# Performance work log

Measured on AMD Instinct MI355X. Metric: run time of the kernel, lower is better.

The kernel has to match this reference:

```python
import jax, jax.numpy as jnp
import numpy as np

N = 100000
E = 2000000
F = 64          # in_features == out_features (required by attention * h_j)
BETA = 0.5
NEG_SLOPE = 0.01  # torch F.leaky_relu default


def setup_inputs() -> dict:
    key = jax.random.key(0)
    k1, k2, k3, k4, k5, k6 = jax.random.split(key, 6)
    h = jax.random.normal(k1, (N, F), dtype=jnp.float32)
    adj = jax.random.randint(k2, (2, E), 0, N, dtype=jnp.int64)
    amount = jax.random.uniform(k3, (E,), dtype=jnp.float32)
    count = jax.random.uniform(k4, (E,), dtype=jnp.float32)
    fc_w = jax.random.normal(k5, (F, 2 * F), dtype=jnp.float32) * (1.0 / np.sqrt(2 * F))
    fc_b = jax.random.normal(k6, (F,), dtype=jnp.float32) * 0.01
    return {"h": h, "adj": adj, "amount": amount, "count": count,
            "fc_w": fc_w, "fc_b": fc_b}


def _minmax_norm(x):
    lo, hi = x.min(), x.max()
    return (x - lo) / (hi - lo + 1e-8)


def reference(h, adj, amount, count, fc_w, fc_b):
    # per-edge weight from normalized amount/count
    edge_weight = BETA * _minmax_norm(amount) + (1.0 - BETA) * _minmax_norm(count)  # [E]

    src, dst = adj[0], adj[1]
    h_i = h[src]                     # [E, F]
    h_j = h[dst]                     # [E, F]
    h_cat = jnp.concatenate([h_i, h_j], axis=1)  # [E, 2F]

    score = jnp.einsum('ef,of->eo', h_cat, fc_w) + fc_b  # [E, F_out]
    score = jnp.where(score >= 0, score, NEG_SLOPE * score)  # leaky_relu
    score = score * edge_weight[:, None]

    # softmax over ALL edges (dim 0), per feature, as in the original
    attention = jax.nn.softmax(score, axis=0)  # [E, F]

    agg = jnp.zeros_like(h).at[src].add(attention * h_j)  # scatter-add -> [N, F]
    return agg
```

## Files before the change

kernel.cpp:

```cpp
#include <hip/hip_runtime.h>
#include <hip/hip_fp16.h>
#include <math.h>

#define FDIM   64
#define NB     128
#define BSHIFT 8
#define BMASK  255
#define EPTA   16
#define CHUNKA (EPTA * 256)
#define DMASK  0xFFFFF
#define MAXBKT 512

__global__ __launch_bounds__(256) void count_mm_k(const int* __restrict__ src,
                                                  const float* __restrict__ amount,
                                                  const float* __restrict__ count,
                                                  int* __restrict__ bktTotal,
                                                  float4* __restrict__ partial,
                                                  int E, int nbkt) {
  __shared__ int lhist[MAXBKT];
  __shared__ float4 lred[4];
  for (int k = threadIdx.x; k < nbkt; k += 256) lhist[k] = 0;
  __syncthreads();
  float amin = 3.4e38f, amax = -3.4e38f, cmin = 3.4e38f, cmax = -3.4e38f;
  int e0 = blockIdx.x * CHUNKA + threadIdx.x * EPTA;
  if (e0 + EPTA <= E) {
    #pragma unroll
    for (int q = 0; q < EPTA; q += 4) {
      int4   s4 = *(const int4*)(src + e0 + q);
      float4 a4 = *(const float4*)(amount + e0 + q);
      float4 c4 = *(const float4*)(count + e0 + q);
      atomicAdd(&lhist[s4.x >> BSHIFT], 1);
      atomicAdd(&lhist[s4.y >> BSHIFT], 1);
      atomicAdd(&lhist[s4.z >> BSHIFT], 1);
      atomicAdd(&lhist[s4.w >> BSHIFT], 1);
      amin = fminf(amin, fminf(fminf(a4.x, a4.y), fminf(a4.z, a4.w)));
      amax = fmaxf(amax, fmaxf(fmaxf(a4.x, a4.y), fmaxf(a4.z, a4.w)));
      cmin = fminf(cmin, fminf(fminf(c4.x, c4.y), fminf(c4.z, c4.w)));
      cmax = fmaxf(cmax, fmaxf(fmaxf(c4.x, c4.y), fmaxf(c4.z, c4.w)));
    }
  } else {
    for (int e = e0; e < E; e++) {
      atomicAdd(&lhist[src[e] >> BSHIFT], 1);
      float a = amount[e], c = count[e];
      amin = fminf(amin, a); amax = fmaxf(amax, a);
      cmin = fminf(cmin, c); cmax = fmaxf(cmax, c);
    }
  }
  #pragma unroll
  for (int off = 32; off; off >>= 1) {
    amin = fminf(amin, __shfl_down(amin, off));
    amax = fmaxf(amax, __shfl_down(amax, off));
    cmin = fminf(cmin, __shfl_down(cmin, off));
    cmax = fmaxf(cmax, __shfl_down(cmax, off));
  }
  if ((threadIdx.x & 63) == 0) lred[threadIdx.x >> 6] = make_float4(amin, amax, cmin, cmax);
  __syncthreads();
  for (int k = threadIdx.x; k < nbkt; k += 256)
    if (lhist[k]) atomicAdd(&bktTotal[k], lhist[k]);
  if (threadIdx.x == 0) {
    float4 r = lred[0];
    #pragma unroll
    for (int w = 1; w < 4; w++) {
      r.x = fminf(r.x, lred[w].x); r.y = fmaxf(r.y, lred[w].y);
      r.z = fminf(r.z, lred[w].z); r.w = fmaxf(r.w, lred[w].w);
    }
    partial[blockIdx.x] = r;
  }
}

__global__ __launch_bounds__(256) void scanB_k(const int* __restrict__ bktTotal,
                                               int* __restrict__ bbase,
                                               int* __restrict__ cursor,
                                               const float4* __restrict__ partial,
                                               float* __restrict__ mmf,
                                               int nbkt, int nb, int E) {
  __shared__ int lds[MAXBKT];
  const int t = threadIdx.x;
  for (int k = t; k < nbkt; k += 256) lds[k] = bktTotal[k];
  __syncthreads();
  __shared__ int tmp[256];
  int running = 0;
  for (int c0 = 0; c0 < nbkt; c0 += 256) {
    int x = (c0 + t < nbkt) ? lds[c0 + t] : 0;
    tmp[t] = x; __syncthreads();
    for (int off = 1; off < 256; off <<= 1) {
      int v = (t >= off) ? tmp[t - off] : 0;
      __syncthreads();
      tmp[t] += v; __syncthreads();
    }
    if (c0 + t < nbkt) {
      int b = running + tmp[t] - x;
      bbase[c0 + t] = b;
      cursor[c0 + t] = b;
    }
    running += tmp[255];
    __syncthreads();
  }
  if (t == 0) bbase[nbkt] = E;
  float amin = 3.4e38f, amax = -3.4e38f, cmin = 3.4e38f, cmax = -3.4e38f;
  for (int i = t; i < nb; i += 256) {
    float4 p = partial[i];
    amin = fminf(amin, p.x); amax = fmaxf(amax, p.y);
    cmin = fminf(cmin, p.z); cmax = fmaxf(cmax, p.w);
  }
  #pragma unroll
  for (int off = 32; off; off >>= 1) {
    amin = fminf(amin, __shfl_down(amin, off));
    amax = fmaxf(amax, __shfl_down(amax, off));
    cmin = fminf(cmin, __shfl_down(cmin, off));
    cmax = fmaxf(cmax, __shfl_down(cmax, off));
  }
  __shared__ float4 lred[4];
  if ((t & 63) == 0) lred[t >> 6] = make_float4(amin, amax, cmin, cmax);
  __syncthreads();
  if (t == 0) {
    float4 r = lred[0];
    #pragma unroll
    for (int w = 1; w < 4; w++) {
      r.x = fminf(r.x, lred[w].x); r.y = fmaxf(r.y, lred[w].y);
      r.z = fminf(r.z, lred[w].z); r.w = fmaxf(r.w, lred[w].w);
    }
    mmf[0] = r.x; mmf[1] = r.y; mmf[2] = r.z; mmf[3] = r.w;
  }
}

__global__ __launch_bounds__(256) void scatter_k(const int* __restrict__ src,
                                                 const int* __restrict__ dst,
                                                 const float* __restrict__ amount,
                                                 const float* __restrict__ count,
                                                 const float* __restrict__ mmf,
                                                 int* __restrict__ cursor,
                                                 int2* __restrict__ payload,
                                                 int E, int nbkt) {
  __shared__ int lhist[MAXBKT];
  __shared__ int lcur[MAXBKT];
  const int t = threadIdx.x;
  for (int k = t; k < nbkt; k += 256) lhist[k] = 0;
  __syncthreads();
  const float amin = mmf[0], amax = mmf[1], cmin = mmf[2], cmax = mmf[3];
  const float L2E = 1.4426950408889634f;
  const float ascale = 0.5f * L2E / (amax - amin + 1e-8f);
  const float cscale = 0.5f * L2E / (cmax - cmin + 1e-8f);
  int e0 = blockIdx.x * CHUNKA + t * EPTA;
  const bool full = (e0 + EPTA <= E);
  int4 S[4]; int4 D[4]; float4 A[4]; float4 C[4];
  if (full) {
    #pragma unroll
    for (int q = 0; q < 4; q++) {
      S[q] = *(const int4*)(src + e0 + 4 * q);
      D[q] = *(const int4*)(dst + e0 + 4 * q);
      A[q] = *(const float4*)(amount + e0 + 4 * q);
      C[q] = *(const float4*)(count + e0 + 4 * q);
      atomicAdd(&lhist[S[q].x >> BSHIFT], 1);
      atomicAdd(&lhist[S[q].y >> BSHIFT], 1);
      atomicAdd(&lhist[S[q].z >> BSHIFT], 1);
      atomicAdd(&lhist[S[q].w >> BSHIFT], 1);
    }
  } else {
    for (int e = e0; e < E; e++) atomicAdd(&lhist[src[e] >> BSHIFT], 1);
  }
  __syncthreads();
  for (int k = t; k < nbkt; k += 256)
    lcur[k] = lhist[k] ? atomicAdd(&cursor[k], lhist[k]) : 0;
  __syncthreads();
  auto ins = [&](int s, int d, float a, float c) {
    int b = s >> BSHIFT;
    float ew = (a - amin) * ascale + (c - cmin) * cscale;
    int pos = atomicAdd(&lcur[b], 1);
    payload[pos] = make_int2(d | ((s & BMASK) << 20), __float_as_int(ew));
  };
  if (full) {
    #pragma unroll
    for (int q = 0; q < 4; q++) {
      ins(S[q].x, D[q].x, A[q].x, C[q].x);
      ins(S[q].y, D[q].y, A[q].y, C[q].y);
      ins(S[q].z, D[q].z, A[q].z, C[q].z);
      ins(S[q].w, D[q].w, A[q].w, C[q].w);
    }
  } else {
    for (int e = e0; e < E; e++) ins(src[e], dst[e], amount[e], count[e]);
  }
}

__global__ __launch_bounds__(256) void binB_k(const int2* __restrict__ payload,
                                              const int* __restrict__ bbase,
                                              int2* __restrict__ edge_s,
                                              int E, int nbkt) {
  __shared__ int fcnt[256];
  __shared__ int tmp[256];
  __shared__ int fcur[256];
  const int b = blockIdx.x;
  const int t = threadIdx.x;
  const int base = bbase[b];
  const int end  = bbase[b + 1];
  fcnt[t] = 0;
  __syncthreads();
  for (int i = base + t; i < end; i += 256)
    atomicAdd(&fcnt[(payload[i].x >> 20) & BMASK], 1);
  __syncthreads();
  int x = fcnt[t];
  tmp[t] = x; __syncthreads();
  for (int off = 1; off < 256; off <<= 1) {
    int v = (t >= off) ? tmp[t - off] : 0;
    __syncthreads();
    tmp[t] += v; __syncthreads();
  }
  fcur[t] = base + tmp[t] - x;
  __syncthreads();
  for (int i = base + t; i < end; i += 256) {
    int2 v = payload[i];
    int pos = atomicAdd(&fcur[(v.x >> 20) & BMASK], 1);
    edge_s[pos] = v;
  }
}

__global__ __launch_bounds__(256) void pre_gemm(const float* __restrict__ h,
                                                const float* __restrict__ fc_w,
                                                const float* __restrict__ fc_b,
                                                float* __restrict__ G1,
                                                __half2* __restrict__ P, int N) {
  __shared__ float hs[NB * FDIM];
  const int t = threadIdx.x;
  const int o = t & 63, half = (t >> 6) & 1, rg = t >> 7;
  float w[FDIM];
  const float* wrow = fc_w + o * 128 + half * 64;
  #pragma unroll
  for (int f = 0; f < FDIM; f += 4) {
    float4 v = *(const float4*)(wrow + f);
    w[f] = v.x; w[f + 1] = v.y; w[f + 2] = v.z; w[f + 3] = v.w;
  }
  const float bias = (half == 0) ? fc_b[o] : 0.0f;
  const int n0 = blockIdx.x * NB;
  const int nrows = min(NB, N - n0);
  {
    const float4* hsrc = (const float4*)(h + (size_t)n0 * FDIM);
    float4* hd = (float4*)hs;
    for (int i = t; i < nrows * (FDIM / 4); i += 256) hd[i] = hsrc[i];
  }
  __syncthreads();
  const int r0 = rg * 64;
  const int r1 = min(r0 + 64, nrows);
  for (int n = r0; n < r1; n++) {
    float acc = bias;
    #pragma unroll
    for (int f = 0; f < FDIM; f += 4) {
      float4 hv = *(const float4*)(&hs[n * FDIM + f]);
      acc += hv.x * w[f] + hv.y * w[f + 1] + hv.z * w[f + 2] + hv.w * w[f + 3];
    }
    if (half == 0) {
      G1[(size_t)(n0 + n) * FDIM + o] = acc;
    } else {
      P[(size_t)(n0 + n) * FDIM + o] =
          __halves2half2(__float2half(acc), __float2half(hs[n * FDIM + o]));
    }
  }
}

__device__ __forceinline__ float2 unpack_h2(unsigned u) {
  __half2 v = *(__half2*)&u;
  return make_float2(__low2float(v), __high2float(v));
}

__global__ __launch_bounds__(256) void fused_k(const int2* __restrict__ edge_s,
                                               const int* __restrict__ bbase,
                                               const float* __restrict__ G1,
                                               const unsigned* __restrict__ P,
                                               double* __restrict__ colsum,
                                               float* __restrict__ out,
                                               int E, int nbkt) {
  const int lane = threadIdx.x & 63;
  const int wv = __builtin_amdgcn_readfirstlane(threadIdx.x >> 6);
  const int wid = blockIdx.x * 4 + wv;
  const int nw = gridDim.x * 4;
  float csum = 0.0f;
  const int per = (((E + nw - 1) / nw) + 63) & ~63;
  const int e0 = wid * per;
  const int e1 = min(e0 + per, E);
  if (e0 < E) {
    int lo = 0, hi = nbkt - 1;
    while (lo < hi) {
      int mid = (lo + hi + 1) >> 1;
      if (bbase[mid] <= e0) lo = mid; else hi = mid - 1;
    }
    int bkt = lo;
    int nextb = bbase[bkt + 1];
    int curnode = -1;
    bool firstf = true;
    float acc = 0.0f, g1 = 0.0f;
    auto flush_to = [&](int node) {
      if (curnode >= 0) {
        float* dp = out + (size_t)curnode * FDIM + lane;
        if (firstf) { atomicAdd(dp, acc); firstf = false; }
        else *dp = acc;
      }
      curnode = node; acc = 0.0f;
      g1 = G1[(size_t)node * FDIM + lane];
    };
    for (int c0 = e0; c0 < e1; c0 += 64) {
      const int m = min(64, e1 - c0);
      int2 p = make_int2(0, 0);
      if (lane < m) p = edge_s[c0 + lane];
      if (m == 64) {
        #pragma unroll 1
        for (int j = 0; j < 64; j += 16) {
          int dd[16], nd[16]; float ee[16]; unsigned uu[16];
          #pragma unroll
          for (int k = 0; k < 16; k++) {
            int x = __builtin_amdgcn_readlane(p.x, j + k);
            ee[k] = __int_as_float(__builtin_amdgcn_readlane(p.y, j + k));
            dd[k] = x & DMASK;
            nd[k] = (x >> 20) & BMASK;
          }
          #pragma unroll
          for (int k = 0; k < 16; k++) uu[k] = P[(size_t)dd[k] * FDIM + lane];
          #pragma unroll
          for (int k = 0; k < 16; k++) {
            int i = c0 + j + k;
            while (i >= nextb) { bkt++; nextb = bbase[bkt + 1]; }
            int node = (bkt << BSHIFT) + nd[k];
            if (node != curnode) flush_to(node);
            float2 v = unpack_h2(uu[k]);
            float sc = g1 + v.x;
            sc = fmaxf(sc, 0.01f * sc);
            float x = exp2f(sc * ee[k]);
            csum += x;
            acc += x * v.y;
          }
        }
      } else {
        for (int j = 0; j < m; j += 16) {
          const int rem = m - j;
          int dd[16], nd[16]; float ee[16]; unsigned uu[16];
          #pragma unroll
          for (int k = 0; k < 16; k++) {
            int x = __builtin_amdgcn_readlane(p.x, j + k);
            ee[k] = __int_as_float(__builtin_amdgcn_readlane(p.y, j + k));
            dd[k] = x & DMASK;
            nd[k] = (x >> 20) & BMASK;
          }
          #pragma unroll
          for (int k = 0; k < 16; k++) uu[k] = P[(size_t)dd[k] * FDIM + lane];
          #pragma unroll
          for (int k = 0; k < 16; k++) {
            if (k < rem) {
              int i = c0 + j + k;
              while (i >= nextb) { bkt++; nextb = bbase[bkt + 1]; }
              int node = (bkt << BSHIFT) + nd[k];
              if (node != curnode) flush_to(node);
              float2 v = unpack_h2(uu[k]);
              float sc = g1 + v.x;
              sc = fmaxf(sc, 0.01f * sc);
              float x = exp2f(sc * ee[k]);
              csum += x;
              acc += x * v.y;
            }
          }
        }
      }
    }
    if (curnode >= 0) atomicAdd(out + (size_t)curnode * FDIM + lane, acc);
  }
  __shared__ float part[256];
  part[threadIdx.x] = csum;
  __syncthreads();
  if (threadIdx.x < 64) {
    float tot = part[threadIdx.x] + part[threadIdx.x + 64] +
                part[threadIdx.x + 128] + part[threadIdx.x + 192];
    atomicAdd(&colsum[threadIdx.x * 16], (double)tot);
  }
}

__global__ __launch_bounds__(256) void scale_k(float4* __restrict__ out4,
                                               const double* __restrict__ colsum,
                                               int total4) {
  __shared__ float rinv_s[64];
  if (threadIdx.x < 64) rinv_s[threadIdx.x] = (float)(1.0 / colsum[threadIdx.x * 16]);
  __syncthreads();
  const float4* r4 = (const float4*)rinv_s;
  int idx = blockIdx.x * blockDim.x + threadIdx.x;
  int stride = gridDim.x * blockDim.x;
  for (int i = idx; i < total4; i += stride) {
    float4 v = out4[i];
    float4 r = r4[i & 15];
    v.x *= r.x; v.y *= r.y; v.z *= r.z; v.w *= r.w;
    out4[i] = v;
  }
}

extern "C" void kernel_launch(void* const* d_in, const int* in_sizes, int n_in,
                              void* d_out, int out_size, void* d_ws, size_t ws_size,
                              hipStream_t stream) {
  const float* h      = (const float*)d_in[0];
  const int*   adj    = (const int*)d_in[1];
  const float* amount = (const float*)d_in[2];
  const float* count  = (const float*)d_in[3];
  const float* fc_w   = (const float*)d_in[4];
  const float* fc_b   = (const float*)d_in[5];
  float* out = (float*)d_out;

  const int E = in_sizes[2];
  const int N = in_sizes[0] / FDIM;
  const int* src = adj;
  const int* dst = adj + E;
  const int nbkt  = (N + BMASK) >> BSHIFT;
  const int nblkA = (E + CHUNKA - 1) / CHUNKA;

  char* ws = (char*)d_ws;
  size_t off = 0;
  auto alloc = [&](size_t bytes) { void* p = ws + off; off += (bytes + 255) & ~(size_t)255; return p; };
  float*    G1       = (float*)alloc((size_t)N * FDIM * sizeof(float));
  __half2*  P        = (__half2*)alloc((size_t)N * FDIM * sizeof(__half2));
  int2*     edge_s   = (int2*)alloc((size_t)E * sizeof(int2));
  int2*     payload  = (int2*)alloc((size_t)E * sizeof(int2));
  char*     ctrl     = (char*)alloc(MAXBKT * sizeof(int) + 1024 * sizeof(double));
  int*      bktTotal = (int*)ctrl;
  double*   colsum   = (double*)(ctrl + MAXBKT * sizeof(int));
  int*      bbase    = (int*)alloc((MAXBKT + 1) * sizeof(int));
  int*      cursor   = (int*)alloc(MAXBKT * sizeof(int));
  float4*   mmpart   = (float4*)alloc((size_t)nblkA * sizeof(float4));
  float*    mmf      = (float*)alloc(4 * sizeof(float));

  hipMemsetAsync(d_out, 0, (size_t)out_size * sizeof(float), stream);
  hipMemsetAsync(ctrl, 0, MAXBKT * sizeof(int) + 1024 * sizeof(double), stream);
  count_mm_k<<<nblkA, 256, 0, stream>>>(src, amount, count, bktTotal, mmpart, E, nbkt);
  scanB_k<<<1, 256, 0, stream>>>(bktTotal, bbase, cursor, mmpart, mmf, nbkt, nblkA, E);
  scatter_k<<<nblkA, 256, 0, stream>>>(src, dst, amount, count, mmf, cursor, payload, E, nbkt);
  binB_k<<<nbkt, 256, 0, stream>>>(payload, bbase, edge_s, E, nbkt);
  pre_gemm<<<(N + NB - 1) / NB, 256, 0, stream>>>(h, fc_w, fc_b, G1, P, N);
  fused_k<<<4096, 256, 0, stream>>>(edge_s, bbase, G1, (const unsigned*)P, colsum, out, E, nbkt);
  scale_k<<<1024, 256, 0, stream>>>((float4*)out, colsum, N * FDIM / 4);
}
```

Measured before the change: 314.2 us.

## Fuse preprocessing into a cooperative kernel and merge binning with pre-GEMM

Replaces the two memsets and the count, scan and scatter kernels with one cooperative kernel that uses grid-wide syncs between phases. The edge data is loaded once and kept in registers across the histogram and scatter phases, so it is no longer re-read. The bucket binning and the pre-GEMM become one launch whose blocks take one role or the other by index. This cuts launch overhead and redundant reads, at the cost of grid.sync latency and a requirement that all nblkA (about 489) blocks be co-resident for the cooperative launch.

```diff
diff --git a/kernel.cpp b/kernel.cpp
--- a/kernel.cpp
+++ b/kernel.cpp
@@ -1,6 +1,9 @@
 #include <hip/hip_runtime.h>
+#include <hip/hip_cooperative_groups.h>
 #include <hip/hip_fp16.h>
 #include <math.h>
+
+namespace cg = cooperative_groups;
 
 #define FDIM   64
 #define NB     128
@@ -11,137 +14,43 @@
 #define DMASK  0xFFFFF
 #define MAXBKT 512
 
-__global__ __launch_bounds__(256) void count_mm_k(const int* __restrict__ src,
-                                                  const float* __restrict__ amount,
-                                                  const float* __restrict__ count,
-                                                  int* __restrict__ bktTotal,
-                                                  float4* __restrict__ partial,
-                                                  int E, int nbkt) {
-  __shared__ int lhist[MAXBKT];
-  __shared__ float4 lred[4];
-  for (int k = threadIdx.x; k < nbkt; k += 256) lhist[k] = 0;
-  __syncthreads();
-  float amin = 3.4e38f, amax = -3.4e38f, cmin = 3.4e38f, cmax = -3.4e38f;
-  int e0 = blockIdx.x * CHUNKA + threadIdx.x * EPTA;
-  if (e0 + EPTA <= E) {
-    #pragma unroll
-    for (int q = 0; q < EPTA; q += 4) {
-      int4   s4 = *(const int4*)(src + e0 + q);
-      float4 a4 = *(const float4*)(amount + e0 + q);
-      float4 c4 = *(const float4*)(count + e0 + q);
-      atomicAdd(&lhist[s4.x >> BSHIFT], 1);
-      atomicAdd(&lhist[s4.y >> BSHIFT], 1);
-      atomicAdd(&lhist[s4.z >> BSHIFT], 1);
-      atomicAdd(&lhist[s4.w >> BSHIFT], 1);
-      amin = fminf(amin, fminf(fminf(a4.x, a4.y), fminf(a4.z, a4.w)));
-      amax = fmaxf(amax, fmaxf(fmaxf(a4.x, a4.y), fmaxf(a4.z, a4.w)));
-      cmin = fminf(cmin, fminf(fminf(c4.x, c4.y), fminf(c4.z, c4.w)));
-      cmax = fmaxf(cmax, fmaxf(fmaxf(c4.x, c4.y), fmaxf(c4.z, c4.w)));
-    }
-  } else {
-    for (int e = e0; e < E; e++) {
-      atomicAdd(&lhist[src[e] >> BSHIFT], 1);
-      float a = amount[e], c = count[e];
-      amin = fminf(amin, a); amax = fmaxf(amax, a);
-      cmin = fminf(cmin, c); cmax = fmaxf(cmax, c);
-    }
-  }
-  #pragma unroll
-  for (int off = 32; off; off >>= 1) {
-    amin = fminf(amin, __shfl_down(amin, off));
-    amax = fmaxf(amax, __shfl_down(amax, off));
-    cmin = fminf(cmin, __shfl_down(cmin, off));
-    cmax = fmaxf(cmax, __shfl_down(cmax, off));
-  }
-  if ((threadIdx.x & 63) == 0) lred[threadIdx.x >> 6] = make_float4(amin, amax, cmin, cmax);
-  __syncthreads();
-  for (int k = threadIdx.x; k < nbkt; k += 256)
-    if (lhist[k]) atomicAdd(&bktTotal[k], lhist[k]);
-  if (threadIdx.x == 0) {
-    float4 r = lred[0];
-    #pragma unroll
-    for (int w = 1; w < 4; w++) {
-      r.x = fminf(r.x, lred[w].x); r.y = fmaxf(r.y, lred[w].y);
-      r.z = fminf(r.z, lred[w].z); r.w = fmaxf(r.w, lred[w].w);
-    }
-    partial[blockIdx.x] = r;
-  }
-}
-
-__global__ __launch_bounds__(256) void scanB_k(const int* __restrict__ bktTotal,
+__global__ __launch_bounds__(256) void build_k(const int* __restrict__ src,
+                                               const int* __restrict__ dst,
+                                               const float* __restrict__ amount,
+                                               const float* __restrict__ count,
+                                               float* __restrict__ out,
+                                               int* __restrict__ bktTotal,
+                                               double* __restrict__ colsum,
                                                int* __restrict__ bbase,
                                                int* __restrict__ cursor,
-                                               const float4* __restrict__ partial,
+                                               float4* __restrict__ partial,
                                                float* __restrict__ mmf,
-                                               int nbkt, int nb, int E) {
-  __shared__ int lds[MAXBKT];
-  const int t = threadIdx.x;
-  for (int k = t; k < nbkt; k += 256) lds[k] = bktTotal[k];
-  __syncthreads();
-  __shared__ int tmp[256];
-  int running = 0;
-  for (int c0 = 0; c0 < nbkt; c0 += 256) {
-    int x = (c0 + t < nbkt) ? lds[c0 + t] : 0;
-    tmp[t] = x; __syncthreads();
-    for (int off = 1; off < 256; off <<= 1) {
-      int v = (t >= off) ? tmp[t - off] : 0;
-      __syncthreads();
-      tmp[t] += v; __syncthreads();
-    }
-    if (c0 + t < nbkt) {
-      int b = running + tmp[t] - x;
-      bbase[c0 + t] = b;
-      cursor[c0 + t] = b;
-    }
-    running += tmp[255];
-    __syncthreads();
-  }
-  if (t == 0) bbase[nbkt] = E;
-  float amin = 3.4e38f, amax = -3.4e38f, cmin = 3.4e38f, cmax = -3.4e38f;
-  for (int i = t; i < nb; i += 256) {
-    float4 p = partial[i];
-    amin = fminf(amin, p.x); amax = fmaxf(amax, p.y);
-    cmin = fminf(cmin, p.z); cmax = fmaxf(cmax, p.w);
-  }
-  #pragma unroll
-  for (int off = 32; off; off >>= 1) {
-    amin = fminf(amin, __shfl_down(amin, off));
-    amax = fmaxf(amax, __shfl_down(amax, off));
-    cmin = fminf(cmin, __shfl_down(cmin, off));
-    cmax = fmaxf(cmax, __shfl_down(cmax, off));
-  }
-  __shared__ float4 lred[4];
-  if ((t & 63) == 0) lred[t >> 6] = make_float4(amin, amax, cmin, cmax);
-  __syncthreads();
-  if (t == 0) {
-    float4 r = lred[0];
-    #pragma unroll
-    for (int w = 1; w < 4; w++) {
-      r.x = fminf(r.x, lred[w].x); r.y = fmaxf(r.y, lred[w].y);
-      r.z = fminf(r.z, lred[w].z); r.w = fmaxf(r.w, lred[w].w);
-    }
-    mmf[0] = r.x; mmf[1] = r.y; mmf[2] = r.z; mmf[3] = r.w;
-  }
-}
-
-__global__ __launch_bounds__(256) void scatter_k(const int* __restrict__ src,
-                                                 const int* __restrict__ dst,
-                                                 const float* __restrict__ amount,
-                                                 const float* __restrict__ count,
-                                                 const float* __restrict__ mmf,
-                                                 int* __restrict__ cursor,
-                                                 int2* __restrict__ payload,
-                                                 int E, int nbkt) {
+                                               int2* __restrict__ payload,
+                                               int E, int N, int nbkt, int nblkA) {
+  cg::grid_group grid = cg::this_grid();
   __shared__ int lhist[MAXBKT];
   __shared__ int lcur[MAXBKT];
+  __shared__ int tmp[256];
+  __shared__ float4 lred[4];
   const int t = threadIdx.x;
+  const int gtid = blockIdx.x * 256 + t;
+  const int nthr = gridDim.x * 256;
+
+  {
+    float4* o4 = (float4*)out;
+    const int tot4 = N * FDIM / 4;
+    const float4 z = make_float4(0.f, 0.f, 0.f, 0.f);
+    for (int i = gtid; i < tot4; i += nthr) o4[i] = z;
+    if (blockIdx.x == 0) {
+      for (int k = t; k < nbkt; k += 256) bktTotal[k] = 0;
+      for (int k = t; k < 1024; k += 256) colsum[k] = 0.0;
+    }
+  }
   for (int k = t; k < nbkt; k += 256) lhist[k] = 0;
-  __syncthreads();
-  const float amin = mmf[0], amax = mmf[1], cmin = mmf[2], cmax = mmf[3];
-  const float L2E = 1.4426950408889634f;
-  const float ascale = 0.5f * L2E / (amax - amin + 1e-8f);
-  const float cscale = 0.5f * L2E / (cmax - cmin + 1e-8f);
-  int e0 = blockIdx.x * CHUNKA + t * EPTA;
+  grid.sync();
+
+  float amin = 3.4e38f, amax = -3.4e38f, cmin = 3.4e38f, cmax = -3.4e38f;
+  const int e0 = blockIdx.x * CHUNKA + t * EPTA;
   const bool full = (e0 + EPTA <= E);
   int4 S[4]; int4 D[4]; float4 A[4]; float4 C[4];
   if (full) {
@@ -155,17 +64,98 @@
       atomicAdd(&lhist[S[q].y >> BSHIFT], 1);
       atomicAdd(&lhist[S[q].z >> BSHIFT], 1);
       atomicAdd(&lhist[S[q].w >> BSHIFT], 1);
+      amin = fminf(amin, fminf(fminf(A[q].x, A[q].y), fminf(A[q].z, A[q].w)));
+      amax = fmaxf(amax, fmaxf(fmaxf(A[q].x, A[q].y), fmaxf(A[q].z, A[q].w)));
+      cmin = fminf(cmin, fminf(fminf(C[q].x, C[q].y), fminf(C[q].z, C[q].w)));
+      cmax = fmaxf(cmax, fmaxf(fmaxf(C[q].x, C[q].y), fmaxf(C[q].z, C[q].w)));
     }
   } else {
-    for (int e = e0; e < E; e++) atomicAdd(&lhist[src[e] >> BSHIFT], 1);
-  }
+    for (int e = e0; e < E; e++) {
+      atomicAdd(&lhist[src[e] >> BSHIFT], 1);
+      float a = amount[e], c = count[e];
+      amin = fminf(amin, a); amax = fmaxf(amax, a);
+      cmin = fminf(cmin, c); cmax = fmaxf(cmax, c);
+    }
+  }
+  #pragma unroll
+  for (int off = 32; off; off >>= 1) {
+    amin = fminf(amin, __shfl_down(amin, off));
+    amax = fmaxf(amax, __shfl_down(amax, off));
+    cmin = fminf(cmin, __shfl_down(cmin, off));
+    cmax = fmaxf(cmax, __shfl_down(cmax, off));
+  }
+  if ((t & 63) == 0) lred[t >> 6] = make_float4(amin, amax, cmin, cmax);
   __syncthreads();
+  for (int k = t; k < nbkt; k += 256)
+    if (lhist[k]) atomicAdd(&bktTotal[k], lhist[k]);
+  if (t == 0) {
+    float4 r = lred[0];
+    #pragma unroll
+    for (int w = 1; w < 4; w++) {
+      r.x = fminf(r.x, lred[w].x); r.y = fmaxf(r.y, lred[w].y);
+      r.z = fminf(r.z, lred[w].z); r.w = fmaxf(r.w, lred[w].w);
+    }
+    partial[blockIdx.x] = r;
+  }
+  grid.sync();
+
+  if (blockIdx.x == 0) {
+    int running = 0;
+    for (int c0 = 0; c0 < nbkt; c0 += 256) {
+      int x = (c0 + t < nbkt) ? bktTotal[c0 + t] : 0;
+      tmp[t] = x; __syncthreads();
+      for (int off = 1; off < 256; off <<= 1) {
+        int v = (t >= off) ? tmp[t - off] : 0;
+        __syncthreads();
+        tmp[t] += v; __syncthreads();
+      }
+      if (c0 + t < nbkt) {
+        int b = running + tmp[t] - x;
+        bbase[c0 + t] = b;
+        cursor[c0 + t] = b;
+      }
+      running += tmp[255];
+      __syncthreads();
+    }
+    if (t == 0) bbase[nbkt] = E;
+    float am = 3.4e38f, ax = -3.4e38f, cm = 3.4e38f, cx = -3.4e38f;
+    for (int i = t; i < nblkA; i += 256) {
+      float4 p = partial[i];
+      am = fminf(am, p.x); ax = fmaxf(ax, p.y);
+      cm = fminf(cm, p.z); cx = fmaxf(cx, p.w);
+    }
+    #pragma unroll
+    for (int off = 32; off; off >>= 1) {
+      am = fminf(am, __shfl_down(am, off));
+      ax = fmaxf(ax, __shfl_down(ax, off));
+      cm = fminf(cm, __shfl_down(cm, off));
+      cx = fmaxf(cx, __shfl_down(cx, off));
+    }
+    __syncthreads();
+    if ((t & 63) == 0) lred[t >> 6] = make_float4(am, ax, cm, cx);
+    __syncthreads();
+    if (t == 0) {
+      float4 r = lred[0];
+      #pragma unroll
+      for (int w = 1; w < 4; w++) {
+        r.x = fminf(r.x, lred[w].x); r.y = fmaxf(r.y, lred[w].y);
+        r.z = fminf(r.z, lred[w].z); r.w = fmaxf(r.w, lred[w].w);
+      }
+      mmf[0] = r.x; mmf[1] = r.y; mmf[2] = r.z; mmf[3] = r.w;
+    }
+  }
+  grid.sync();
+
+  const float famin = mmf[0], famax = mmf[1], fcmin = mmf[2], fcmax = mmf[3];
+  const float L2E = 1.4426950408889634f;
+  const float ascale = 0.5f * L2E / (famax - famin + 1e-8f);
+  const float cscale = 0.5f * L2E / (fcmax - fcmin + 1e-8f);
   for (int k = t; k < nbkt; k += 256)
     lcur[k] = lhist[k] ? atomicAdd(&cursor[k], lhist[k]) : 0;
   __syncthreads();
   auto ins = [&](int s, int d, float a, float c) {
     int b = s >> BSHIFT;
-    float ew = (a - amin) * ascale + (c - cmin) * cscale;
+    float ew = (a - famin) * ascale + (c - fcmin) * cscale;
     int pos = atomicAdd(&lcur[b], 1);
     payload[pos] = make_int2(d | ((s & BMASK) << 20), __float_as_int(ew));
   };
@@ -182,76 +172,76 @@
   }
 }
 
-__global__ __launch_bounds__(256) void binB_k(const int2* __restrict__ payload,
-                                              const int* __restrict__ bbase,
-                                              int2* __restrict__ edge_s,
-                                              int E, int nbkt) {
-  __shared__ int fcnt[256];
-  __shared__ int tmp[256];
-  __shared__ int fcur[256];
-  const int b = blockIdx.x;
-  const int t = threadIdx.x;
-  const int base = bbase[b];
-  const int end  = bbase[b + 1];
-  fcnt[t] = 0;
-  __syncthreads();
-  for (int i = base + t; i < end; i += 256)
-    atomicAdd(&fcnt[(payload[i].x >> 20) & BMASK], 1);
-  __syncthreads();
-  int x = fcnt[t];
-  tmp[t] = x; __syncthreads();
-  for (int off = 1; off < 256; off <<= 1) {
-    int v = (t >= off) ? tmp[t - off] : 0;
-    __syncthreads();
-    tmp[t] += v; __syncthreads();
-  }
-  fcur[t] = base + tmp[t] - x;
-  __syncthreads();
-  for (int i = base + t; i < end; i += 256) {
-    int2 v = payload[i];
-    int pos = atomicAdd(&fcur[(v.x >> 20) & BMASK], 1);
-    edge_s[pos] = v;
-  }
-}
-
-__global__ __launch_bounds__(256) void pre_gemm(const float* __restrict__ h,
-                                                const float* __restrict__ fc_w,
-                                                const float* __restrict__ fc_b,
-                                                float* __restrict__ G1,
-                                                __half2* __restrict__ P, int N) {
+__global__ __launch_bounds__(256) void binB_pre_k(const int2* __restrict__ payload,
+                                                  const int* __restrict__ bbase,
+                                                  int2* __restrict__ edge_s,
+                                                  const float* __restrict__ h,
+                                                  const float* __restrict__ fc_w,
+                                                  const float* __restrict__ fc_b,
+                                                  float* __restrict__ G1,
+                                                  __half2* __restrict__ P,
+                                                  int E, int nbkt, int N) {
   __shared__ float hs[NB * FDIM];
   const int t = threadIdx.x;
-  const int o = t & 63, half = (t >> 6) & 1, rg = t >> 7;
-  float w[FDIM];
-  const float* wrow = fc_w + o * 128 + half * 64;
-  #pragma unroll
-  for (int f = 0; f < FDIM; f += 4) {
-    float4 v = *(const float4*)(wrow + f);
-    w[f] = v.x; w[f + 1] = v.y; w[f + 2] = v.z; w[f + 3] = v.w;
-  }
-  const float bias = (half == 0) ? fc_b[o] : 0.0f;
-  const int n0 = blockIdx.x * NB;
-  const int nrows = min(NB, N - n0);
-  {
-    const float4* hsrc = (const float4*)(h + (size_t)n0 * FDIM);
-    float4* hd = (float4*)hs;
-    for (int i = t; i < nrows * (FDIM / 4); i += 256) hd[i] = hsrc[i];
-  }
-  __syncthreads();
-  const int r0 = rg * 64;
-  const int r1 = min(r0 + 64, nrows);
-  for (int n = r0; n < r1; n++) {
-    float acc = bias;
+  if ((int)blockIdx.x < nbkt) {
+    int* fcnt = (int*)hs;
+    int* tmp  = fcnt + 256;
+    int* fcur = tmp + 256;
+    const int b = blockIdx.x;
+    const int base = bbase[b];
+    const int end  = bbase[b + 1];
+    fcnt[t] = 0;
+    __syncthreads();
+    for (int i = base + t; i < end; i += 256)
+      atomicAdd(&fcnt[(payload[i].x >> 20) & BMASK], 1);
+    __syncthreads();
+    int x = fcnt[t];
+    tmp[t] = x; __syncthreads();
+    for (int off = 1; off < 256; off <<= 1) {
+      int v = (t >= off) ? tmp[t - off] : 0;
+      __syncthreads();
+      tmp[t] += v; __syncthreads();
+    }
+    fcur[t] = base + tmp[t] - x;
+    __syncthreads();
+    for (int i = base + t; i < end; i += 256) {
+      int2 v = payload[i];
+      int pos = atomicAdd(&fcur[(v.x >> 20) & BMASK], 1);
+      edge_s[pos] = v;
+    }
+  } else {
+    const int o = t & 63, half = (t >> 6) & 1, rg = t >> 7;
+    float w[FDIM];
+    const float* wrow = fc_w + o * 128 + half * 64;
     #pragma unroll
     for (int f = 0; f < FDIM; f += 4) {
-      float4 hv = *(const float4*)(&hs[n * FDIM + f]);
-      acc += hv.x * w[f] + hv.y * w[f + 1] + hv.z * w[f + 2] + hv.w * w[f + 3];
-    }
-    if (half == 0) {
-      G1[(size_t)(n0 + n) * FDIM + o] = acc;
-    } else {
-      P[(size_t)(n0 + n) * FDIM + o] =
-          __halves2half2(__float2half(acc), __float2half(hs[n * FDIM + o]));
+      float4 v = *(const float4*)(wrow + f);
+      w[f] = v.x; w[f + 1] = v.y; w[f + 2] = v.z; w[f + 3] = v.w;
+    }
+    const float bias = (half == 0) ? fc_b[o] : 0.0f;
+    const int n0 = (blockIdx.x - nbkt) * NB;
+    const int nrows = min(NB, N - n0);
+    {
+      const float4* hsrc = (const float4*)(h + (size_t)n0 * FDIM);
+      float4* hd = (float4*)hs;
+      for (int i = t; i < nrows * (FDIM / 4); i += 256) hd[i] = hsrc[i];
+    }
+    __syncthreads();
+    const int r0 = rg * 64;
+    const int r1 = min(r0 + 64, nrows);
+    for (int n = r0; n < r1; n++) {
+      float acc = bias;
+      #pragma unroll
+      for (int f = 0; f < FDIM; f += 4) {
+        float4 hv = *(const float4*)(&hs[n * FDIM + f]);
+        acc += hv.x * w[f] + hv.y * w[f + 1] + hv.z * w[f + 2] + hv.w * w[f + 3];
+      }
+      if (half == 0) {
+        G1[(size_t)(n0 + n) * FDIM + o] = acc;
+      } else {
+        P[(size_t)(n0 + n) * FDIM + o] =
+            __halves2half2(__float2half(acc), __float2half(hs[n * FDIM + o]));
+      }
     }
   }
 }
@@ -412,21 +402,22 @@
   __half2*  P        = (__half2*)alloc((size_t)N * FDIM * sizeof(__half2));
   int2*     edge_s   = (int2*)alloc((size_t)E * sizeof(int2));
   int2*     payload  = (int2*)alloc((size_t)E * sizeof(int2));
-  char*     ctrl     = (char*)alloc(MAXBKT * sizeof(int) + 1024 * sizeof(double));
-  int*      bktTotal = (int*)ctrl;
-  double*   colsum   = (double*)(ctrl + MAXBKT * sizeof(int));
+  int*      bktTotal = (int*)alloc(MAXBKT * sizeof(int));
+  double*   colsum   = (double*)alloc(1024 * sizeof(double));
   int*      bbase    = (int*)alloc((MAXBKT + 1) * sizeof(int));
   int*      cursor   = (int*)alloc(MAXBKT * sizeof(int));
   float4*   mmpart   = (float4*)alloc((size_t)nblkA * sizeof(float4));
   float*    mmf      = (float*)alloc(4 * sizeof(float));
 
-  hipMemsetAsync(d_out, 0, (size_t)out_size * sizeof(float), stream);
-  hipMemsetAsync(ctrl, 0, MAXBKT * sizeof(int) + 1024 * sizeof(double), stream);
-  count_mm_k<<<nblkA, 256, 0, stream>>>(src, amount, count, bktTotal, mmpart, E, nbkt);
-  scanB_k<<<1, 256, 0, stream>>>(bktTotal, bbase, cursor, mmpart, mmf, nbkt, nblkA, E);
-  scatter_k<<<nblkA, 256, 0, stream>>>(src, dst, amount, count, mmf, cursor, payload, E, nbkt);
-  binB_k<<<nbkt, 256, 0, stream>>>(payload, bbase, edge_s, E, nbkt);
-  pre_gemm<<<(N + NB - 1) / NB, 256, 0, stream>>>(h, fc_w, fc_b, G1, P, N);
+  {
+    void* args[] = {(void*)&src, (void*)&dst, (void*)&amount, (void*)&count,
+                    (void*)&out, (void*)&bktTotal, (void*)&colsum, (void*)&bbase,
+                    (void*)&cursor, (void*)&mmpart, (void*)&mmf, (void*)&payload,
+                    (void*)&E, (void*)&N, (void*)&nbkt, (void*)&nblkA};
+    hipLaunchCooperativeKernel((void*)build_k, dim3(nblkA), dim3(256), args, 0, stream);
+  }
+  binB_pre_k<<<nbkt + (N + NB - 1) / NB, 256, 0, stream>>>(
+      payload, bbase, edge_s, h, fc_w, fc_b, G1, P, E, nbkt, N);
   fused_k<<<4096, 256, 0, stream>>>(edge_s, bbase, G1, (const unsigned*)P, colsum, out, E, nbkt);
   scale_k<<<1024, 256, 0, stream>>>((float4*)out, colsum, N * FDIM / 4);
 }
```

Measured after the change: 467.5 us. +48.8%, slower.
